# Kernel optimization log

Measured on AMD Instinct MI355X. Metric: run time of the kernel, lower is better.

The kernel has to match this reference:

```python
import jax, jax.numpy as jnp
import numpy as np
import math

HID, NH, NKV, HD = 2048, 16, 4, 128
GROUPS = NH // NKV
ROPE_THETA = 10000.0
NBITS = 8


def fake_quant(x, n_bits=NBITS):
    """Per-tensor symmetric min-max fake quantization with STE."""
    qmax = float(2 ** (n_bits - 1) - 1)
    scale = jnp.maximum(jnp.max(jnp.abs(x)) / qmax, jnp.asarray(1e-8, x.dtype))
    q = jnp.clip(jnp.round(x / scale), -qmax - 1.0, qmax) * scale
    return x + jax.lax.stop_gradient(q - x)


def quant_linear(x, w):
    # QuantLinear: fake-quant activation and weight, then x @ w.T
    return jnp.einsum('bsh,oh->bso', fake_quant(x), fake_quant(w))


def rope_cos_sin(position_ids, head_dim, dtype):
    inv_freq = 1.0 / (ROPE_THETA ** (jnp.arange(0, head_dim, 2, dtype=jnp.float32) / head_dim))
    freqs = position_ids.astype(jnp.float32)[..., None] * inv_freq  # [B,S,hd/2]
    emb = jnp.concatenate([freqs, freqs], axis=-1)                   # [B,S,hd]
    return jnp.cos(emb).astype(dtype), jnp.sin(emb).astype(dtype)


def rotate_half(x):
    h = x.shape[-1] // 2
    return jnp.concatenate([-x[..., h:], x[..., :h]], axis=-1)


def setup_inputs() -> dict:
    key = jax.random.key(0)
    ks = jax.random.split(key, 6)
    B, S = 2, 2048
    hidden_states = jax.random.normal(ks[0], (B, S, HID), dtype=jnp.float32)
    neg = jnp.finfo(jnp.float32).min
    causal = jnp.where(jnp.tril(jnp.ones((S, S), dtype=bool)), 0.0, neg).astype(jnp.float32)
    attention_mask = jnp.broadcast_to(causal[None, None], (B, 1, S, S))
    position_ids = jnp.broadcast_to(jnp.arange(S, dtype=jnp.int64)[None], (B, S))
    wq = jax.random.normal(ks[1], (NH * HD, HID), dtype=jnp.float32) * 0.02
    wk = jax.random.normal(ks[2], (NKV * HD, HID), dtype=jnp.float32) * 0.02
    wv = jax.random.normal(ks[3], (NKV * HD, HID), dtype=jnp.float32) * 0.02
    wo = jax.random.normal(ks[4], (HID, NH * HD), dtype=jnp.float32) * 0.02
    return {"hidden_states": hidden_states, "attention_mask": attention_mask,
            "position_ids": position_ids, "wq": wq, "wk": wk, "wv": wv, "wo": wo}


def reference(hidden_states, attention_mask, position_ids, wq, wk, wv, wo):
    B, S, _ = hidden_states.shape
    dtype = hidden_states.dtype
    # quantized projections -> [B, nH, S, hd] / [B, nKV, S, hd]
    q = quant_linear(hidden_states, wq).reshape(B, S, NH, HD).transpose(0, 2, 1, 3)
    k = quant_linear(hidden_states, wk).reshape(B, S, NKV, HD).transpose(0, 2, 1, 3)
    v = quant_linear(hidden_states, wv).reshape(B, S, NKV, HD).transpose(0, 2, 1, 3)
    # RoPE
    cos, sin = rope_cos_sin(position_ids, HD, dtype)
    cos, sin = cos[:, None], sin[:, None]  # broadcast over heads
    q = q * cos + rotate_half(q) * sin
    k = k * cos + rotate_half(k) * sin
    # repeat_kv (GQA)
    k = jnp.repeat(k, GROUPS, axis=1)
    v = jnp.repeat(v, GROUPS, axis=1)
    # fake-quantized QK^T
    q = fake_quant(q)
    k = fake_quant(k)
    attn_weights = jnp.einsum('bhqd,bhkd->bhqk', q, k) / math.sqrt(HD)
    attn_weights = attn_weights + attention_mask
    attn_weights = jnp.maximum(attn_weights, jnp.finfo(attn_weights.dtype).min)
    attn_weights = jax.nn.softmax(attn_weights.astype(jnp.float32), axis=-1).astype(dtype)
    # fake-quantized PV
    p = fake_quant(attn_weights)
    v = fake_quant(v)
    attn_output = jnp.einsum('bhqk,bhkd->bhqd', p, v)
    attn_output = attn_output.transpose(0, 2, 1, 3).reshape(B, S, NH * HD)
    return quant_linear(attn_output, wo)
```

## Files before the change

### kernel.cpp

```cpp
#include <hip/hip_runtime.h>
#include <math.h>
#include <stdint.h>
#include <stddef.h>

#define HID 2048
#define NH 16
#define NKV 4
#define HD 128
#define GROUPS (NH / NKV)
#define BATCH 2
#define SEQ 2048

#define N_HS  8388608ull
#define N_Q   8388608ull
#define N_KV  2097152ull
#define N_WQ  4194304ull
#define N_WKV 1048576ull
#define N_WO  4194304ull

typedef __attribute__((ext_vector_type(8))) short bf16x8;
typedef __attribute__((ext_vector_type(4))) float f32x4;

#define LOG2E 1.4426950408889634f
#define CLAMP_L2 115.41560325f

__device__ inline float quantv(float x, float s) {
  float q = rintf(x / s);
  return fminf(fmaxf(q, -128.0f), 127.0f);
}

__device__ inline float slot_scale(const unsigned int* slots, int i) {
  return fmaxf(__uint_as_float(slots[i]) / 127.0f, 1e-8f);
}

__device__ inline unsigned short f2bf(float x) {
  return (unsigned short)(__float_as_uint(x) >> 16);
}

__device__ inline float amax4(float4 v) {
  return fmaxf(fmaxf(fabsf(v.x), fabsf(v.y)), fmaxf(fabsf(v.z), fabsf(v.w)));
}

__device__ inline void block_amax_atomic(float m, unsigned int* slot) {
  __shared__ float red[256];
  red[threadIdx.x] = m;
  __syncthreads();
  for (int o = 128; o > 0; o >>= 1) {
    if (threadIdx.x < o) red[threadIdx.x] = fmaxf(red[threadIdx.x], red[threadIdx.x + o]);
    __syncthreads();
  }
  if (threadIdx.x == 0) atomicMax(slot, __float_as_uint(red[0]));
}

__device__ __forceinline__ void gload_lds16(const void* g, void* l) {
  __builtin_amdgcn_global_load_lds((const __attribute__((address_space(1))) unsigned int*)g,
                                   (__attribute__((address_space(3))) unsigned int*)l, 16, 0, 0);
}

__global__ __launch_bounds__(256) void absmax5_k(const float* __restrict__ a0,
                                                 const float* __restrict__ a1,
                                                 const float* __restrict__ a2,
                                                 const float* __restrict__ a3,
                                                 const float* __restrict__ a4,
                                                 unsigned int* __restrict__ slots) {
  const int t = blockIdx.y;
  const float* x = t == 0 ? a0 : t == 1 ? a1 : t == 2 ? a2 : t == 3 ? a3 : a4;
  const size_t n4 = (t == 0 ? N_HS : t == 1 ? N_WQ : t == 2 ? N_WKV : t == 3 ? N_WKV : N_WO) / 4;
  const float4* xp = (const float4*)x;
  float m = 0.0f;
  for (size_t i = (size_t)blockIdx.x * 256 + threadIdx.x; i < n4; i += (size_t)gridDim.x * 256)
    m = fmaxf(m, amax4(xp[i]));
  block_amax_atomic(m, slots + t);
}

__global__ __launch_bounds__(256) void quant5_k(const float* __restrict__ a0,
                                                const float* __restrict__ a1,
                                                const float* __restrict__ a2,
                                                const float* __restrict__ a3,
                                                const float* __restrict__ a4,
                                                const unsigned int* __restrict__ slots,
                                                unsigned short* __restrict__ o0,
                                                unsigned short* __restrict__ o1,
                                                unsigned short* __restrict__ o2,
                                                unsigned short* __restrict__ o3,
                                                unsigned short* __restrict__ o4) {
  const int t = blockIdx.y;
  const float* x = t == 0 ? a0 : t == 1 ? a1 : t == 2 ? a2 : t == 3 ? a3 : a4;
  unsigned short* o = t == 0 ? o0 : t == 1 ? o1 : t == 2 ? o2 : t == 3 ? o3 : o4;
  const size_t n4 = (t == 0 ? N_HS : t == 1 ? N_WQ : t == 2 ? N_WKV : t == 3 ? N_WKV : N_WO) / 4;
  const float s = fmaxf(__uint_as_float(slots[t]) / 127.0f, 1e-8f);
  const float4* xp = (const float4*)x;
  ushort4* op = (ushort4*)o;
  for (size_t i = (size_t)blockIdx.x * 256 + threadIdx.x; i < n4; i += (size_t)gridDim.x * 256) {
    float4 v = xp[i];
    ushort4 r;
    r.x = f2bf(quantv(v.x, s));
    r.y = f2bf(quantv(v.y, s));
    r.z = f2bf(quantv(v.z, s));
    r.w = f2bf(quantv(v.w, s));
    op[i] = r;
  }
}

__global__ __launch_bounds__(256) void quant2_k(const float* __restrict__ a0,
                                                const float* __restrict__ a1,
                                                const unsigned int* __restrict__ slots,
                                                unsigned short* __restrict__ o0,
                                                unsigned short* __restrict__ o1) {
  const int t = blockIdx.y;
  const float* x = t == 0 ? a0 : a1;
  unsigned short* o = t == 0 ? o0 : o1;
  const size_t n4 = (t == 0 ? N_Q : N_KV) / 4;
  const float s = fmaxf(__uint_as_float(slots[5 + t]) / 127.0f, 1e-8f);
  const float4* xp = (const float4*)x;
  ushort4* op = (ushort4*)o;
  for (size_t i = (size_t)blockIdx.x * 256 + threadIdx.x; i < n4; i += (size_t)gridDim.x * 256) {
    float4 v = xp[i];
    ushort4 r;
    r.x = f2bf(quantv(v.x, s));
    r.y = f2bf(quantv(v.y, s));
    r.z = f2bf(quantv(v.z, s));
    r.w = f2bf(quantv(v.w, s));
    op[i] = r;
  }
}

__global__ __launch_bounds__(256) void quant1_k(const float* __restrict__ x, size_t n4,
                                                const unsigned int* __restrict__ slot,
                                                unsigned short* __restrict__ out) {
  const float s = fmaxf(__uint_as_float(*slot) / 127.0f, 1e-8f);
  const float4* xp = (const float4*)x;
  ushort4* op = (ushort4*)out;
  for (size_t i = (size_t)blockIdx.x * 256 + threadIdx.x; i < n4; i += (size_t)gridDim.x * 256) {
    float4 v = xp[i];
    ushort4 r;
    r.x = f2bf(quantv(v.x, s));
    r.y = f2bf(quantv(v.y, s));
    r.z = f2bf(quantv(v.z, s));
    r.w = f2bf(quantv(v.w, s));
    op[i] = r;
  }
}

__global__ __launch_bounds__(256) void vtq_k(const float* __restrict__ vbuf,
                                             const unsigned int* __restrict__ slots,
                                             unsigned short* __restrict__ vbt) {
  __shared__ unsigned short L[128 * 72];
  const int tid = threadIdx.x;
  const int s0 = blockIdx.x * 64;
  const int hk = blockIdx.y;
  const int b = blockIdx.z;
  const float s = fmaxf(__uint_as_float(slots[7]) / 127.0f, 1e-8f);
#pragma unroll
  for (int it = 0; it < 8; it++) {
    int idx = tid + it * 256;
    int sl = idx >> 5, c4 = idx & 31;
    float4 v = ((const float4*)(vbuf + ((size_t)(b * SEQ + s0 + sl) * NKV + hk) * HD))[c4];
    L[(c4 * 4 + 0) * 72 + sl] = f2bf(quantv(v.x, s));
    L[(c4 * 4 + 1) * 72 + sl] = f2bf(quantv(v.y, s));
    L[(c4 * 4 + 2) * 72 + sl] = f2bf(quantv(v.z, s));
    L[(c4 * 4 + 3) * 72 + sl] = f2bf(quantv(v.w, s));
  }
  __syncthreads();
  const size_t obase = ((size_t)(b * NKV + hk)) * HD * SEQ + s0;
#pragma unroll
  for (int it = 0; it < 4; it++) {
    int idx = tid + it * 256;
    int d = idx >> 3, sc = idx & 7;
    *(bf16x8*)(vbt + obase + (size_t)d * SEQ + sc * 8) = *(const bf16x8*)(&L[d * 72 + sc * 8]);
  }
}

__device__ __forceinline__ void gemm_body(const unsigned short* __restrict__ A,
                                          const unsigned short* __restrict__ B,
                                          float* __restrict__ C, int N, int K, int m0, int n0,
                                          float sc, int amax_slot, unsigned int* slots) {
  __shared__ unsigned short As[3][128 * 32];
  __shared__ unsigned short Bs[3][128 * 32];
  const int tid = threadIdx.x;
  const int wave = tid >> 6, lane = tid & 63;
  const int l16 = lane & 15, quad = lane >> 4;
  const int wm = (wave & 1) * 64, wn = (wave >> 1) * 64;

  f32x4 acc[4][4];
#pragma unroll
  for (int i = 0; i < 4; i++)
#pragma unroll
    for (int j = 0; j < 4; j++) acc[i][j] = (f32x4){0.f, 0.f, 0.f, 0.f};

  auto STAGE = [&](int buf, int kt) {
#pragma unroll
    for (int it = 0; it < 2; it++) {
      int c = it * 256 + tid;
      int r = c >> 2, kc = (c & 3) * 8;
      gload_lds16(A + (size_t)(m0 + r) * K + kt + kc, &As[buf][(it * 256 + wave * 64) * 8]);
      gload_lds16(B + (size_t)(n0 + r) * K + kt + kc, &Bs[buf][(it * 256 + wave * 64) * 8]);
    }
  };

  const int nk = K / 32;
  STAGE(0, 0);
  STAGE(1, 32);
  STAGE(2, 64);
  for (int t = 0; t < nk; t++) {
    const int buf = t % 3;
    if (t + 3 < nk + 1)      asm volatile("s_waitcnt vmcnt(8)" ::: "memory");
    else if (t + 2 < nk + 1) asm volatile("s_waitcnt vmcnt(4)" ::: "memory");
    else                     asm volatile("s_waitcnt vmcnt(0)" ::: "memory");
    __builtin_amdgcn_sched_barrier(0);
    __builtin_amdgcn_s_barrier();
    __builtin_amdgcn_sched_barrier(0);
    bf16x8 af[4], bq[4];
#pragma unroll
    for (int i = 0; i < 4; i++)
      af[i] = *(const bf16x8*)(&As[buf][(wm + i * 16 + l16) * 32 + quad * 8]);
#pragma unroll
    for (int j = 0; j < 4; j++)
      bq[j] = *(const bf16x8*)(&Bs[buf][(wn + j * 16 + l16) * 32 + quad * 8]);
    asm volatile("s_waitcnt lgkmcnt(0)" ::: "memory");
    __builtin_amdgcn_sched_barrier(0);
    __builtin_amdgcn_s_barrier();
    __builtin_amdgcn_sched_barrier(0);
    if (t + 3 < nk) STAGE(buf, (t + 3) * 32);
#pragma unroll
    for (int i = 0; i < 4; i++)
#pragma unroll
      for (int j = 0; j < 4; j++)
        acc[i][j] = __builtin_amdgcn_mfma_f32_16x16x32_bf16(af[i], bq[j], acc[i][j], 0, 0, 0);
  }

  float am = 0.0f;
#pragma unroll
  for (int i = 0; i < 4; i++)
#pragma unroll
    for (int j = 0; j < 4; j++)
#pragma unroll
      for (int r = 0; r < 4; r++) {
        int row = m0 + wm + i * 16 + quad * 4 + r;
        int col = n0 + wn + j * 16 + l16;
        float v = acc[i][j][r] * sc;
        C[(size_t)row * N + col] = v;
        am = fmaxf(am, fabsf(v));
      }
  if (amax_slot >= 0) {
    __syncthreads();
    float* red = (float*)As;
    red[tid] = am;
    __syncthreads();
    for (int o = 128; o > 0; o >>= 1) {
      if (tid < o) red[tid] = fmaxf(red[tid], red[tid + o]);
      __syncthreads();
    }
    if (tid == 0) atomicMax(slots + amax_slot, __float_as_uint(red[0]));
  }
}

__global__ __launch_bounds__(256) void gemm_qkv_k(const unsigned short* __restrict__ A,
                                                  const unsigned short* __restrict__ Bq,
                                                  const unsigned short* __restrict__ Bk,
                                                  const unsigned short* __restrict__ Bv,
                                                  float* __restrict__ Cq, float* __restrict__ Ck,
                                                  float* __restrict__ Cv,
                                                  unsigned int* __restrict__ slots) {
  const int nt = blockIdx.x, m0 = blockIdx.y * 128;
  const unsigned short* B;
  float* C;
  int N, n0, ib, amx;
  if (nt < 16) {
    B = Bq; C = Cq; N = 2048; n0 = nt * 128; ib = 1; amx = -1;
  } else if (nt < 20) {
    B = Bk; C = Ck; N = 512; n0 = (nt - 16) * 128; ib = 2; amx = -1;
  } else {
    B = Bv; C = Cv; N = 512; n0 = (nt - 20) * 128; ib = 3; amx = 7;
  }
  const float sc = slot_scale(slots, 0) * slot_scale(slots, ib);
  gemm_body(A, B, C, N, HID, m0, n0, sc, amx, slots);
}

__global__ __launch_bounds__(256) void gemm_o_k(const unsigned short* __restrict__ A,
                                                const unsigned short* __restrict__ B,
                                                float* __restrict__ C,
                                                unsigned int* __restrict__ slots) {
  const float sc = slot_scale(slots, 8) * slot_scale(slots, 4);
  gemm_body(A, B, C, HID, NH * HD, blockIdx.y * 128, blockIdx.x * 128, sc, -1, slots);
}

__global__ __launch_bounds__(256) void rope_table_k(float2* __restrict__ tab) {
  int idx = blockIdx.x * 256 + threadIdx.x;
  int i = idx & 63, s = idx >> 6;
  float inv = 1.0f / powf(10000.0f, (float)(2 * i) * (1.0f / 128.0f));
  float fr = (float)s * inv;
  tab[idx] = make_float2(cosf(fr), sinf(fr));
}

__global__ __launch_bounds__(256) void rope_kernel(float* __restrict__ t, int nh, int nhs,
                                                   const float2* __restrict__ tab,
                                                   unsigned int* __restrict__ slot) {
  const size_t total4 = (size_t)BATCH * SEQ * nh * 16;
  float am = 0.0f;
  for (size_t it = (size_t)blockIdx.x * 256 + threadIdx.x; it < total4;
       it += (size_t)gridDim.x * 256) {
    const int i4 = (int)(it & 15);
    const int h = (int)((it >> 4) & (nh - 1));
    const int s = (int)((it >> (4 + nhs)) & (SEQ - 1));
    const int b = (int)(it >> (15 + nhs));
    const size_t base = ((size_t)(b * SEQ + s) * nh + h) * HD + i4 * 4;
    float4 x1 = *(const float4*)(t + base);
    float4 x2 = *(const float4*)(t + base + 64);
    const float4* tp = (const float4*)(tab + (s << 6) + i4 * 4);
    float4 cs01 = tp[0];
    float4 cs23 = tp[1];
    float4 r1, r2;
    r1.x = x1.x * cs01.x - x2.x * cs01.y;  r2.x = x2.x * cs01.x + x1.x * cs01.y;
    r1.y = x1.y * cs01.z - x2.y * cs01.w;  r2.y = x2.y * cs01.z + x1.y * cs01.w;
    r1.z = x1.z * cs23.x - x2.z * cs23.y;  r2.z = x2.z * cs23.x + x1.z * cs23.y;
    r1.w = x1.w * cs23.z - x2.w * cs23.w;  r2.w = x2.w * cs23.z + x1.w * cs23.w;
    *(float4*)(t + base) = r1;
    *(float4*)(t + base + 64) = r2;
    am = fmaxf(am, fmaxf(amax4(r1), amax4(r2)));
  }
  block_amax_atomic(am, slot);
}

#define TK 64
#define KS_STRIDE (HD + 8)
#define VT_STRIDE (TK + 8)
#define PS_STRIDE (TK + 8)

__device__ __forceinline__ void ldK(bf16x8 r[4], const unsigned short* kb, int b, int hk,
                                    int j0, int tid) {
#pragma unroll
  for (int it = 0; it < 4; it++) {
    int c2 = tid + it * 256;
    int rr = c2 >> 4, c = c2 & 15;
    r[it] = *(const bf16x8*)(kb + ((size_t)(b * SEQ + j0 + rr) * NKV + hk) * HD + c * 8);
  }
}
__device__ __forceinline__ void stK(unsigned short* Ks, const bf16x8 r[4], int tid) {
#pragma unroll
  for (int it = 0; it < 4; it++) {
    int c2 = tid + it * 256;
    int rr = c2 >> 4, c = c2 & 15;
    *(bf16x8*)(&Ks[rr * KS_STRIDE + c * 8]) = r[it];
  }
}
__device__ __forceinline__ void ldV(bf16x8 r[4], const unsigned short* vbt, size_t vbase,
                                    int j0, int tid) {
#pragma unroll
  for (int it = 0; it < 4; it++) {
    int idx = tid + it * 256;
    int d = idx >> 3, sc = idx & 7;
    r[it] = *(const bf16x8*)(vbt + vbase + (size_t)d * SEQ + j0 + sc * 8);
  }
}
__device__ __forceinline__ void stV(unsigned short* Vt, const bf16x8 r[4], int tid) {
#pragma unroll
  for (int it = 0; it < 4; it++) {
    int idx = tid + it * 256;
    int d = idx >> 3, sc = idx & 7;
    *(bf16x8*)(&Vt[d * VT_STRIDE + sc * 8]) = r[it];
  }
}

__device__ __forceinline__ void qk4_pair(f32x4 sfrA[4], f32x4 sfrB[4], const unsigned short* Ks,
                                         const bf16x8 qfA[4], const bf16x8 qfB[4], bool doA,
                                         int l16, int quad) {
#pragma unroll
  for (int kt = 0; kt < 4; kt++) {
    f32x4 aA = {0.f, 0.f, 0.f, 0.f}, aB = {0.f, 0.f, 0.f, 0.f};
    const unsigned short* kp = &Ks[(kt * 16 + l16) * KS_STRIDE + quad * 8];
#pragma unroll
    for (int s = 0; s < 4; s++) {
      bf16x8 kf = *(const bf16x8*)(kp + s * 32);
      if (doA) aA = __builtin_amdgcn_mfma_f32_16x16x32_bf16(kf, qfA[s], aA, 0, 0, 0);
      aB = __builtin_amdgcn_mfma_f32_16x16x32_bf16(kf, qfB[s], aB, 0, 0, 0);
    }
    sfrA[kt] = aA;
    sfrB[kt] = aB;
  }
}
__device__ __forceinline__ void lacc(float& l, const f32x4 sfr[4], float c1, bool diag,
                                     int j0, int qrow, int quad) {
  if (!diag) {
#pragma unroll
    for (int kt = 0; kt < 4; kt++)
#pragma unroll
      for (int r = 0; r < 4; r++)
        l += __builtin_amdgcn_exp2f(fminf(sfr[kt][r] * c1, CLAMP_L2));
  } else {
#pragma unroll
    for (int kt = 0; kt < 4; kt++) {
      const int key0 = j0 + kt * 16 + quad * 4;
#pragma unroll
      for (int r = 0; r < 4; r++) {
        float e = __builtin_amdgcn_exp2f(fminf(sfr[kt][r] * c1, CLAMP_L2));
        l += (key0 + r <= qrow) ? e : 0.0f;
      }
    }
  }
}
__device__ __forceinline__ void pquant(unsigned short* Psb, const f32x4 sfr[4],
                                       float l2il, float c1, bool diag, int j0,
                                       int qrow, int wave, int l16, int quad) {
  unsigned short* rowp = &Psb[(wave * 16 + l16) * PS_STRIDE + quad * 4];
#pragma unroll
  for (int kt = 0; kt < 4; kt++) {
    const int key0 = j0 + kt * 16 + quad * 4;
    float p0 = rintf(__builtin_amdgcn_exp2f(fminf(sfr[kt][0] * c1, CLAMP_L2) + l2il));
    float p1 = rintf(__builtin_amdgcn_exp2f(fminf(sfr[kt][1] * c1, CLAMP_L2) + l2il));
    float p2 = rintf(__builtin_amdgcn_exp2f(fminf(sfr[kt][2] * c1, CLAMP_L2) + l2il));
    float p3 = rintf(__builtin_amdgcn_exp2f(fminf(sfr[kt][3] * c1, CLAMP_L2) + l2il));
    if (diag) {
      if (key0 + 0 > qrow) p0 = 0.0f;
      if (key0 + 1 > qrow) p1 = 0.0f;
      if (key0 + 2 > qrow) p2 = 0.0f;
      if (key0 + 3 > qrow) p3 = 0.0f;
    }
    ushort4 pk;
    pk.x = f2bf(p0);
    pk.y = f2bf(p1);
    pk.z = f2bf(p2);
    pk.w = f2bf(p3);
    *(ushort4*)(rowp + kt * 16) = pk;
  }
}
__device__ __forceinline__ void pvacc_pair(f32x4 ofA[8], f32x4 ofB[8], const unsigned short* Ps,
                                           const unsigned short* Vt, bool doA, int wave,
                                           int l16, int quad) {
  const unsigned short* ppA = &Ps[(wave * 16 + l16) * PS_STRIDE + quad * 8];
  const unsigned short* ppB = ppA + 64 * PS_STRIDE;
  bf16x8 pA0, pA1;
  if (doA) {
    pA0 = *(const bf16x8*)ppA;
    pA1 = *(const bf16x8*)(ppA + 32);
  }
  bf16x8 pB0 = *(const bf16x8*)ppB;
  bf16x8 pB1 = *(const bf16x8*)(ppB + 32);
#pragma unroll
  for (int n = 0; n < 8; n++) {
    const unsigned short* vp = &Vt[(n * 16 + l16) * VT_STRIDE + quad * 8];
    bf16x8 v0 = *(const bf16x8*)vp;
    bf16x8 v1 = *(const bf16x8*)(vp + 32);
    ofB[n] = __builtin_amdgcn_mfma_f32_16x16x32_bf16(pB0, v0, ofB[n], 0, 0, 0);
    ofB[n] = __builtin_amdgcn_mfma_f32_16x16x32_bf16(pB1, v1, ofB[n], 0, 0, 0);
    if (doA) {
      ofA[n] = __builtin_amdgcn_mfma_f32_16x16x32_bf16(pA0, v0, ofA[n], 0, 0, 0);
      ofA[n] = __builtin_amdgcn_mfma_f32_16x16x32_bf16(pA1, v1, ofA[n], 0, 0, 0);
    }
  }
}

__global__ __launch_bounds__(256, 2) void attn_mfma_kernel(const unsigned short* __restrict__ qb,
                                                           const unsigned short* __restrict__ kb,
                                                           const unsigned short* __restrict__ vbt,
                                                           float* __restrict__ ob,
                                                           unsigned int* __restrict__ slots) {
  __shared__ unsigned short Ks[TK * KS_STRIDE];
  __shared__ unsigned short Vt[HD * VT_STRIDE];
  __shared__ unsigned short Ps[128 * PS_STRIDE];

  const int tid = threadIdx.x;
  const int wave = tid >> 6;
  const int lane = tid & 63;
  const int l16 = lane & 15;
  const int quad = lane >> 4;
  const int id = blockIdx.x;
  const int b = (id & 7) >> 2;
  const int hk = id & 3;
  const int j = id >> 3;
  const int h = hk * GROUPS + (j & 3);
  const int slot = j >> 2;
  const int q0A = slot * 64, ntA = slot + 1;
  const int q0B = (31 - slot) * 64, ntB = 32 - slot;

  const float s_q = slot_scale(slots, 5);
  const float s_k = slot_scale(slots, 6);
  const float s_v = slot_scale(slots, 7);
  const float ss = s_q * s_k / 11.313708498984761f;
  const float c1 = ss * LOG2E;
  const float scale_p = 1.0f / 127.0f;
  const size_t vbase = ((size_t)(b * NKV + hk)) * HD * SEQ;

  bf16x8 qfA[4], qfB[4];
  {
    const unsigned short* qpA =
        qb + ((size_t)(b * SEQ + q0A + wave * 16 + l16) * NH + h) * HD + quad * 8;
    const unsigned short* qpB =
        qb + ((size_t)(b * SEQ + q0B + wave * 16 + l16) * NH + h) * HD + quad * 8;
#pragma unroll
    for (int s = 0; s < 4; s++) {
      qfA[s] = *(const bf16x8*)(qpA + s * 32);
      qfB[s] = *(const bf16x8*)(qpB + s * 32);
    }
  }
  const int qrowA = q0A + wave * 16 + l16;
  const int qrowB = q0B + wave * 16 + l16;
  const int qrbA = q0A + wave * 16 + quad * 4;
  const int qrbB = q0B + wave * 16 + quad * 4;

  float lA = 0.f, lB = 0.f;
  bf16x8 kreg[4];
  ldK(kreg, kb, b, hk, 0, tid);
  for (int t = 0; t < ntB; t++) {
    const int j0 = t * TK;
    __syncthreads();
    stK(Ks, kreg, tid);
    if (t + 1 < ntB) ldK(kreg, kb, b, hk, (t + 1) * TK, tid);
    __syncthreads();
    const bool doA = (t < ntA);
    f32x4 sfrA[4], sfrB[4];
    qk4_pair(sfrA, sfrB, Ks, qfA, qfB, doA, l16, quad);
    if (doA) lacc(lA, sfrA, c1, t == ntA - 1, j0, qrowA, quad);
    lacc(lB, sfrB, c1, t == ntB - 1, j0, qrowB, quad);
  }
  lA += __shfl_xor(lA, 16);
  lA += __shfl_xor(lA, 32);
  lB += __shfl_xor(lB, 16);
  lB += __shfl_xor(lB, 32);
  const float l2ilA = __log2f(127.0f / fmaxf(lA, 1e-30f));
  const float l2ilB = __log2f(127.0f / fmaxf(lB, 1e-30f));

  f32x4 ofA[8], ofB[8];
#pragma unroll
  for (int n = 0; n < 8; n++) {
    ofA[n] = (f32x4){0.f, 0.f, 0.f, 0.f};
    ofB[n] = (f32x4){0.f, 0.f, 0.f, 0.f};
  }
  bf16x8 vreg[4];
  ldK(kreg, kb, b, hk, 0, tid);
  ldV(vreg, vbt, vbase, 0, tid);
  for (int t = 0; t < ntB; t++) {
    const int j0 = t * TK;
    __syncthreads();
    stK(Ks, kreg, tid);
    stV(Vt, vreg, tid);
    if (t + 1 < ntB) {
      ldK(kreg, kb, b, hk, (t + 1) * TK, tid);
      ldV(vreg, vbt, vbase, (t + 1) * TK, tid);
    }
    __syncthreads();
    const bool doA = (t < ntA);
    f32x4 sfrA[4], sfrB[4];
    qk4_pair(sfrA, sfrB, Ks, qfA, qfB, doA, l16, quad);
    if (doA) pquant(Ps, sfrA, l2ilA, c1, t == ntA - 1, j0, qrowA, wave, l16, quad);
    pquant(Ps + 64 * PS_STRIDE, sfrB, l2ilB, c1, t == ntB - 1, j0, qrowB, wave, l16, quad);
    pvacc_pair(ofA, ofB, Ps, Vt, doA, wave, l16, quad);
  }

  const float oscale = scale_p * s_v;
  float amax = 0.0f;
#pragma unroll
  for (int n = 0; n < 8; n++)
#pragma unroll
    for (int r = 0; r < 4; r++) {
      float vA = ofA[n][r] * oscale;
      float vB = ofB[n][r] * oscale;
      ob[((size_t)(b * SEQ + qrbA + r) * NH + h) * HD + n * 16 + l16] = vA;
      ob[((size_t)(b * SEQ + qrbB + r) * NH + h) * HD + n * 16 + l16] = vB;
      amax = fmaxf(amax, fmaxf(fabsf(vA), fabsf(vB)));
    }
  __syncthreads();
  block_amax_atomic(amax, &slots[8]);
}

extern "C" void kernel_launch(void* const* d_in, const int* in_sizes, int n_in,
                              void* d_out, int out_size, void* d_ws, size_t ws_size,
                              hipStream_t stream) {
  const float* hs = (const float*)d_in[0];
  const float* wq = (const float*)d_in[3];
  const float* wk = (const float*)d_in[4];
  const float* wv = (const float*)d_in[5];
  const float* wo = (const float*)d_in[6];
  float* out = (float*)d_out;

  unsigned int* slots = (unsigned int*)d_ws;
  char* p = (char*)d_ws + 256;
  unsigned short* hsq = (unsigned short*)p;  p += 2 * N_HS;
  unsigned short* wqq = (unsigned short*)p;  p += 2 * N_WQ;
  unsigned short* wkq = (unsigned short*)p;  p += 2 * N_WKV;
  unsigned short* wvq = (unsigned short*)p;  p += 2 * N_WKV;
  unsigned short* woq = (unsigned short*)p;  p += 2 * N_WO;
  float* kbuf = (float*)p;                   p += 4 * N_KV;
  float* vbuf = (float*)p;                   p += 4 * N_KV;
  unsigned short* qbf = (unsigned short*)p;  p += 2 * N_Q;
  unsigned short* kbf = (unsigned short*)p;  p += 2 * N_KV;
  unsigned short* vbt = (unsigned short*)p;  p += 2 * N_KV;
  float2* rtab = (float2*)p;
  unsigned short* aobf = hsq;
  float* qbuf = out;
  float* aobuf = out;

  hipMemsetAsync(d_ws, 0, 256, stream);

  rope_table_k<<<(SEQ * 64) / 256, 256, 0, stream>>>(rtab);
  absmax5_k<<<dim3(256, 5), 256, 0, stream>>>(hs, wq, wk, wv, wo, slots);
  quant5_k<<<dim3(256, 5), 256, 0, stream>>>(hs, wq, wk, wv, wo, slots, hsq, wqq, wkq, wvq, woq);

  const int M = BATCH * SEQ;
  gemm_qkv_k<<<dim3(24, M / 128), 256, 0, stream>>>(hsq, wqq, wkq, wvq, qbuf, kbuf, vbuf, slots);

  rope_kernel<<<1024, 256, 0, stream>>>(qbuf, NH, 4, rtab, slots + 5);
  rope_kernel<<<256, 256, 0, stream>>>(kbuf, NKV, 2, rtab, slots + 6);

  quant2_k<<<dim3(256, 2), 256, 0, stream>>>(qbuf, kbuf, slots, qbf, kbf);
  vtq_k<<<dim3(SEQ / 64, NKV, BATCH), 256, 0, stream>>>(vbuf, slots, vbt);

  attn_mfma_kernel<<<dim3(512, 1, 1), 256, 0, stream>>>(qbf, kbf, vbt, aobuf, slots);

  quant1_k<<<256, 256, 0, stream>>>(aobuf, N_Q / 4, slots + 8, aobf);

  gemm_o_k<<<dim3(HID / 128, M / 128), 256, 0, stream>>>(aobf, woq, out, slots);
}
```

Measured before the change: 416.4 us.

## Split paired causal q-tiles into one tile per block with heavy-first ordering

```diff
diff --git a/kernel.cpp b/kernel.cpp
--- a/kernel.cpp
+++ b/kernel.cpp
@@ -362,21 +362,17 @@
   }
 }
 
-__device__ __forceinline__ void qk4_pair(f32x4 sfrA[4], f32x4 sfrB[4], const unsigned short* Ks,
-                                         const bf16x8 qfA[4], const bf16x8 qfB[4], bool doA,
-                                         int l16, int quad) {
+__device__ __forceinline__ void qk41(f32x4 sfr[4], const unsigned short* Ks,
+                                     const bf16x8 qf[4], int l16, int quad) {
 #pragma unroll
   for (int kt = 0; kt < 4; kt++) {
-    f32x4 aA = {0.f, 0.f, 0.f, 0.f}, aB = {0.f, 0.f, 0.f, 0.f};
+    f32x4 a = {0.f, 0.f, 0.f, 0.f};
     const unsigned short* kp = &Ks[(kt * 16 + l16) * KS_STRIDE + quad * 8];
 #pragma unroll
-    for (int s = 0; s < 4; s++) {
-      bf16x8 kf = *(const bf16x8*)(kp + s * 32);
-      if (doA) aA = __builtin_amdgcn_mfma_f32_16x16x32_bf16(kf, qfA[s], aA, 0, 0, 0);
-      aB = __builtin_amdgcn_mfma_f32_16x16x32_bf16(kf, qfB[s], aB, 0, 0, 0);
-    }
-    sfrA[kt] = aA;
-    sfrB[kt] = aB;
+    for (int s = 0; s < 4; s++)
+      a = __builtin_amdgcn_mfma_f32_16x16x32_bf16(*(const bf16x8*)(kp + s * 32), qf[s], a,
+                                                  0, 0, 0);
+    sfr[kt] = a;
   }
 }
 __device__ __forceinline__ void lacc(float& l, const f32x4 sfr[4], float c1, bool diag,
@@ -424,40 +420,28 @@
     *(ushort4*)(rowp + kt * 16) = pk;
   }
 }
-__device__ __forceinline__ void pvacc_pair(f32x4 ofA[8], f32x4 ofB[8], const unsigned short* Ps,
-                                           const unsigned short* Vt, bool doA, int wave,
-                                           int l16, int quad) {
-  const unsigned short* ppA = &Ps[(wave * 16 + l16) * PS_STRIDE + quad * 8];
-  const unsigned short* ppB = ppA + 64 * PS_STRIDE;
-  bf16x8 pA0, pA1;
-  if (doA) {
-    pA0 = *(const bf16x8*)ppA;
-    pA1 = *(const bf16x8*)(ppA + 32);
-  }
-  bf16x8 pB0 = *(const bf16x8*)ppB;
-  bf16x8 pB1 = *(const bf16x8*)(ppB + 32);
+__device__ __forceinline__ void pvacc1(f32x4 of[8], const unsigned short* Ps,
+                                       const unsigned short* Vt, int wave, int l16, int quad) {
+  const unsigned short* pp = &Ps[(wave * 16 + l16) * PS_STRIDE + quad * 8];
+  bf16x8 p0 = *(const bf16x8*)pp;
+  bf16x8 p1 = *(const bf16x8*)(pp + 32);
 #pragma unroll
   for (int n = 0; n < 8; n++) {
     const unsigned short* vp = &Vt[(n * 16 + l16) * VT_STRIDE + quad * 8];
-    bf16x8 v0 = *(const bf16x8*)vp;
-    bf16x8 v1 = *(const bf16x8*)(vp + 32);
-    ofB[n] = __builtin_amdgcn_mfma_f32_16x16x32_bf16(pB0, v0, ofB[n], 0, 0, 0);
-    ofB[n] = __builtin_amdgcn_mfma_f32_16x16x32_bf16(pB1, v1, ofB[n], 0, 0, 0);
-    if (doA) {
-      ofA[n] = __builtin_amdgcn_mfma_f32_16x16x32_bf16(pA0, v0, ofA[n], 0, 0, 0);
-      ofA[n] = __builtin_amdgcn_mfma_f32_16x16x32_bf16(pA1, v1, ofA[n], 0, 0, 0);
-    }
-  }
-}
-
-__global__ __launch_bounds__(256, 2) void attn_mfma_kernel(const unsigned short* __restrict__ qb,
+    of[n] = __builtin_amdgcn_mfma_f32_16x16x32_bf16(p0, *(const bf16x8*)vp, of[n], 0, 0, 0);
+    of[n] = __builtin_amdgcn_mfma_f32_16x16x32_bf16(p1, *(const bf16x8*)(vp + 32), of[n],
+                                                    0, 0, 0);
+  }
+}
+
+__global__ __launch_bounds__(256, 3) void attn_mfma_kernel(const unsigned short* __restrict__ qb,
                                                            const unsigned short* __restrict__ kb,
                                                            const unsigned short* __restrict__ vbt,
                                                            float* __restrict__ ob,
                                                            unsigned int* __restrict__ slots) {
   __shared__ unsigned short Ks[TK * KS_STRIDE];
   __shared__ unsigned short Vt[HD * VT_STRIDE];
-  __shared__ unsigned short Ps[128 * PS_STRIDE];
+  __shared__ unsigned short Ps[64 * PS_STRIDE];
 
   const int tid = threadIdx.x;
   const int wave = tid >> 6;
@@ -469,9 +453,8 @@
   const int hk = id & 3;
   const int j = id >> 3;
   const int h = hk * GROUPS + (j & 3);
-  const int slot = j >> 2;
-  const int q0A = slot * 64, ntA = slot + 1;
-  const int q0B = (31 - slot) * 64, ntB = 32 - slot;
+  const int tile = 31 - (j >> 2);
+  const int q0 = tile * 64, nt = tile + 1;
 
   const float s_q = slot_scale(slots, 5);
   const float s_k = slot_scale(slots, 6);
@@ -481,70 +464,53 @@
   const float scale_p = 1.0f / 127.0f;
   const size_t vbase = ((size_t)(b * NKV + hk)) * HD * SEQ;
 
-  bf16x8 qfA[4], qfB[4];
+  bf16x8 qf[4];
   {
-    const unsigned short* qpA =
-        qb + ((size_t)(b * SEQ + q0A + wave * 16 + l16) * NH + h) * HD + quad * 8;
-    const unsigned short* qpB =
-        qb + ((size_t)(b * SEQ + q0B + wave * 16 + l16) * NH + h) * HD + quad * 8;
-#pragma unroll
-    for (int s = 0; s < 4; s++) {
-      qfA[s] = *(const bf16x8*)(qpA + s * 32);
-      qfB[s] = *(const bf16x8*)(qpB + s * 32);
-    }
-  }
-  const int qrowA = q0A + wave * 16 + l16;
-  const int qrowB = q0B + wave * 16 + l16;
-  const int qrbA = q0A + wave * 16 + quad * 4;
-  const int qrbB = q0B + wave * 16 + quad * 4;
-
-  float lA = 0.f, lB = 0.f;
+    const unsigned short* qp =
+        qb + ((size_t)(b * SEQ + q0 + wave * 16 + l16) * NH + h) * HD + quad * 8;
+#pragma unroll
+    for (int s = 0; s < 4; s++) qf[s] = *(const bf16x8*)(qp + s * 32);
+  }
+  const int qrow = q0 + wave * 16 + l16;
+  const int qrb = q0 + wave * 16 + quad * 4;
+
+  float l = 0.f;
   bf16x8 kreg[4];
   ldK(kreg, kb, b, hk, 0, tid);
-  for (int t = 0; t < ntB; t++) {
+  for (int t = 0; t < nt; t++) {
     const int j0 = t * TK;
     __syncthreads();
     stK(Ks, kreg, tid);
-    if (t + 1 < ntB) ldK(kreg, kb, b, hk, (t + 1) * TK, tid);
-    __syncthreads();
-    const bool doA = (t < ntA);
-    f32x4 sfrA[4], sfrB[4];
-    qk4_pair(sfrA, sfrB, Ks, qfA, qfB, doA, l16, quad);
-    if (doA) lacc(lA, sfrA, c1, t == ntA - 1, j0, qrowA, quad);
-    lacc(lB, sfrB, c1, t == ntB - 1, j0, qrowB, quad);
-  }
-  lA += __shfl_xor(lA, 16);
-  lA += __shfl_xor(lA, 32);
-  lB += __shfl_xor(lB, 16);
-  lB += __shfl_xor(lB, 32);
-  const float l2ilA = __log2f(127.0f / fmaxf(lA, 1e-30f));
-  const float l2ilB = __log2f(127.0f / fmaxf(lB, 1e-30f));
-
-  f32x4 ofA[8], ofB[8];
-#pragma unroll
-  for (int n = 0; n < 8; n++) {
-    ofA[n] = (f32x4){0.f, 0.f, 0.f, 0.f};
-    ofB[n] = (f32x4){0.f, 0.f, 0.f, 0.f};
-  }
+    if (t + 1 < nt) ldK(kreg, kb, b, hk, (t + 1) * TK, tid);
+    __syncthreads();
+    f32x4 sfr[4];
+    qk41(sfr, Ks, qf, l16, quad);
+    lacc(l, sfr, c1, t == nt - 1, j0, qrow, quad);
+  }
+  l += __shfl_xor(l, 16);
+  l += __shfl_xor(l, 32);
+  const float l2il = __log2f(127.0f / fmaxf(l, 1e-30f));
+
+  f32x4 of[8];
+#pragma unroll
+  for (int n = 0; n < 8; n++) of[n] = (f32x4){0.f, 0.f, 0.f, 0.f};
   bf16x8 vreg[4];
   ldK(kreg, kb, b, hk, 0, tid);
   ldV(vreg, vbt, vbase, 0, tid);
-  for (int t = 0; t < ntB; t++) {
+  for (int t = 0; t < nt; t++) {
     const int j0 = t * TK;
     __syncthreads();
     stK(Ks, kreg, tid);
     stV(Vt, vreg, tid);
-    if (t + 1 < ntB) {
+    if (t + 1 < nt) {
       ldK(kreg, kb, b, hk, (t + 1) * TK, tid);
       ldV(vreg, vbt, vbase, (t + 1) * TK, tid);
     }
     __syncthreads();
-    const bool doA = (t < ntA);
-    f32x4 sfrA[4], sfrB[4];
-    qk4_pair(sfrA, sfrB, Ks, qfA, qfB, doA, l16, quad);
-    if (doA) pquant(Ps, sfrA, l2ilA, c1, t == ntA - 1, j0, qrowA, wave, l16, quad);
-    pquant(Ps + 64 * PS_STRIDE, sfrB, l2ilB, c1, t == ntB - 1, j0, qrowB, wave, l16, quad);
-    pvacc_pair(ofA, ofB, Ps, Vt, doA, wave, l16, quad);
+    f32x4 sfr[4];
+    qk41(sfr, Ks, qf, l16, quad);
+    pquant(Ps, sfr, l2il, c1, t == nt - 1, j0, qrow, wave, l16, quad);
+    pvacc1(of, Ps, Vt, wave, l16, quad);
   }
 
   const float oscale = scale_p * s_v;
@@ -553,14 +519,19 @@
   for (int n = 0; n < 8; n++)
 #pragma unroll
     for (int r = 0; r < 4; r++) {
-      float vA = ofA[n][r] * oscale;
-      float vB = ofB[n][r] * oscale;
-      ob[((size_t)(b * SEQ + qrbA + r) * NH + h) * HD + n * 16 + l16] = vA;
-      ob[((size_t)(b * SEQ + qrbB + r) * NH + h) * HD + n * 16 + l16] = vB;
-      amax = fmaxf(amax, fmaxf(fabsf(vA), fabsf(vB)));
+      float v = of[n][r] * oscale;
+      ob[((size_t)(b * SEQ + qrb + r) * NH + h) * HD + n * 16 + l16] = v;
+      amax = fmaxf(amax, fabsf(v));
     }
   __syncthreads();
-  block_amax_atomic(amax, &slots[8]);
+  float* red = (float*)Ps;
+  red[tid] = amax;
+  __syncthreads();
+  for (int o = 128; o > 0; o >>= 1) {
+    if (tid < o) red[tid] = fmaxf(red[tid], red[tid + o]);
+    __syncthreads();
+  }
+  if (tid == 0) atomicMax(slots + 8, __float_as_uint(red[0]));
 }
 
 extern "C" void kernel_launch(void* const* d_in, const int* in_sizes, int n_in,
@@ -605,7 +576,7 @@
   quant2_k<<<dim3(256, 2), 256, 0, stream>>>(qbuf, kbuf, slots, qbf, kbf);
   vtq_k<<<dim3(SEQ / 64, NKV, BATCH), 256, 0, stream>>>(vbuf, slots, vbt);
 
-  attn_mfma_kernel<<<dim3(512, 1, 1), 256, 0, stream>>>(qbf, kbf, vbt, aobuf, slots);
+  attn_mfma_kernel<<<dim3(1024, 1, 1), 256, 0, stream>>>(qbf, kbf, vbt, aobuf, slots);
 
   quant1_k<<<256, 256, 0, stream>>>(aobuf, N_Q / 4, slots + 8, aobf);
 
```

New measurement: 412.7 us. About the same (-0.9%).

## Pair adjacent 64-row query tiles per block and raise attention occupancy

Applied to the files above, without the earlier changes.

```diff
diff --git a/kernel.cpp b/kernel.cpp
--- a/kernel.cpp
+++ b/kernel.cpp
@@ -450,7 +450,7 @@
   }
 }
 
-__global__ __launch_bounds__(256, 2) void attn_mfma_kernel(const unsigned short* __restrict__ qb,
+__global__ __launch_bounds__(256, 3) void attn_mfma_kernel(const unsigned short* __restrict__ qb,
                                                            const unsigned short* __restrict__ kb,
                                                            const unsigned short* __restrict__ vbt,
                                                            float* __restrict__ ob,
@@ -467,11 +467,11 @@
   const int id = blockIdx.x;
   const int b = (id & 7) >> 2;
   const int hk = id & 3;
-  const int j = id >> 3;
-  const int h = hk * GROUPS + (j & 3);
-  const int slot = j >> 2;
-  const int q0A = slot * 64, ntA = slot + 1;
-  const int q0B = (31 - slot) * 64, ntB = 32 - slot;
+  const int h = hk * GROUPS + ((id >> 3) & 3);
+  const int j5 = id >> 5;
+  const int bt = j5 < 8 ? 15 - j5 : j5 - 8;
+  const int q0 = bt * 128;
+  const int nt = 2 * bt + 2;
 
   const float s_q = slot_scale(slots, 5);
   const float s_k = slot_scale(slots, 6);
@@ -484,34 +484,33 @@
   bf16x8 qfA[4], qfB[4];
   {
     const unsigned short* qpA =
-        qb + ((size_t)(b * SEQ + q0A + wave * 16 + l16) * NH + h) * HD + quad * 8;
-    const unsigned short* qpB =
-        qb + ((size_t)(b * SEQ + q0B + wave * 16 + l16) * NH + h) * HD + quad * 8;
+        qb + ((size_t)(b * SEQ + q0 + wave * 16 + l16) * NH + h) * HD + quad * 8;
+    const unsigned short* qpB = qpA + (size_t)64 * NH * HD;
 #pragma unroll
     for (int s = 0; s < 4; s++) {
       qfA[s] = *(const bf16x8*)(qpA + s * 32);
       qfB[s] = *(const bf16x8*)(qpB + s * 32);
     }
   }
-  const int qrowA = q0A + wave * 16 + l16;
-  const int qrowB = q0B + wave * 16 + l16;
-  const int qrbA = q0A + wave * 16 + quad * 4;
-  const int qrbB = q0B + wave * 16 + quad * 4;
+  const int qrowA = q0 + wave * 16 + l16;
+  const int qrowB = qrowA + 64;
+  const int qrbA = q0 + wave * 16 + quad * 4;
+  const int qrbB = qrbA + 64;
 
   float lA = 0.f, lB = 0.f;
   bf16x8 kreg[4];
   ldK(kreg, kb, b, hk, 0, tid);
-  for (int t = 0; t < ntB; t++) {
+  for (int t = 0; t < nt; t++) {
     const int j0 = t * TK;
     __syncthreads();
     stK(Ks, kreg, tid);
-    if (t + 1 < ntB) ldK(kreg, kb, b, hk, (t + 1) * TK, tid);
-    __syncthreads();
-    const bool doA = (t < ntA);
+    if (t + 1 < nt) ldK(kreg, kb, b, hk, (t + 1) * TK, tid);
+    __syncthreads();
+    const bool doA = (t < nt - 1);
     f32x4 sfrA[4], sfrB[4];
     qk4_pair(sfrA, sfrB, Ks, qfA, qfB, doA, l16, quad);
-    if (doA) lacc(lA, sfrA, c1, t == ntA - 1, j0, qrowA, quad);
-    lacc(lB, sfrB, c1, t == ntB - 1, j0, qrowB, quad);
+    if (doA) lacc(lA, sfrA, c1, t == nt - 2, j0, qrowA, quad);
+    lacc(lB, sfrB, c1, t == nt - 1, j0, qrowB, quad);
   }
   lA += __shfl_xor(lA, 16);
   lA += __shfl_xor(lA, 32);
@@ -529,21 +528,21 @@
   bf16x8 vreg[4];
   ldK(kreg, kb, b, hk, 0, tid);
   ldV(vreg, vbt, vbase, 0, tid);
-  for (int t = 0; t < ntB; t++) {
+  for (int t = 0; t < nt; t++) {
     const int j0 = t * TK;
     __syncthreads();
     stK(Ks, kreg, tid);
     stV(Vt, vreg, tid);
-    if (t + 1 < ntB) {
+    if (t + 1 < nt) {
       ldK(kreg, kb, b, hk, (t + 1) * TK, tid);
       ldV(vreg, vbt, vbase, (t + 1) * TK, tid);
     }
     __syncthreads();
-    const bool doA = (t < ntA);
+    const bool doA = (t < nt - 1);
     f32x4 sfrA[4], sfrB[4];
     qk4_pair(sfrA, sfrB, Ks, qfA, qfB, doA, l16, quad);
-    if (doA) pquant(Ps, sfrA, l2ilA, c1, t == ntA - 1, j0, qrowA, wave, l16, quad);
-    pquant(Ps + 64 * PS_STRIDE, sfrB, l2ilB, c1, t == ntB - 1, j0, qrowB, wave, l16, quad);
+    if (doA) pquant(Ps, sfrA, l2ilA, c1, t == nt - 2, j0, qrowA, wave, l16, quad);
+    pquant(Ps + 64 * PS_STRIDE, sfrB, l2ilB, c1, t == nt - 1, j0, qrowB, wave, l16, quad);
     pvacc_pair(ofA, ofB, Ps, Vt, doA, wave, l16, quad);
   }
 
@@ -560,7 +559,14 @@
       amax = fmaxf(amax, fmaxf(fabsf(vA), fabsf(vB)));
     }
   __syncthreads();
-  block_amax_atomic(amax, &slots[8]);
+  float* red = (float*)Ps;
+  red[tid] = amax;
+  __syncthreads();
+  for (int o = 128; o > 0; o >>= 1) {
+    if (tid < o) red[tid] = fmaxf(red[tid], red[tid + o]);
+    __syncthreads();
+  }
+  if (tid == 0) atomicMax(slots + 8, __float_as_uint(red[0]));
 }
 
 extern "C" void kernel_launch(void* const* d_in, const int* in_sizes, int n_in,
```

After: 497.4 us. 1.19x slower.
